# Performance work log

Measured on AMD Instinct MI355X. Metric: run time of the kernel, lower is better.

## Reference

```python
import jax, jax.numpy as jnp
import numpy as np

B, N, NS, D, H = 32, 4096, 16, 512, 8
DH = D // H          # dims_per_head = 64
DFF = 4 * D          # ff_mlp hidden
SCALE = DH ** -0.5
EPS = 1e-8           # slot-attention renorm eps
LN_EPS = 1e-5        # torch LayerNorm default
ITERS = 3


def layer_norm(x, g, b):
    mu = jnp.mean(x, axis=-1, keepdims=True)
    var = jnp.mean((x - mu) ** 2, axis=-1, keepdims=True)
    return (x - mu) * jax.lax.rsqrt(var + LN_EPS) * g + b


def setup_inputs() -> dict:
    key = jax.random.key(0)
    ks = jax.random.split(key, 8)
    s = 0.02
    return {
        "inputs": jax.random.normal(ks[0], (B, N, D), jnp.float32),
        "conditioning": jax.random.normal(ks[1], (B, NS, D), jnp.float32),
        # norm_input
        "ln_in_g": jnp.ones((D,), jnp.float32),
        "ln_in_b": jnp.zeros((D,), jnp.float32),
        # projections (no bias: use_projection_bias=False)
        "Wk": jax.random.normal(ks[2], (D, D), jnp.float32) * s,
        "Wv": jax.random.normal(ks[3], (D, D), jnp.float32) * s,
        "Wq": jax.random.normal(ks[4], (D, D), jnp.float32) * s,
        "Wo": jax.random.normal(ks[5], (D, D), jnp.float32) * s,
        # norm_slots / norm_slots_ff_mlp
        "ln_s_g": jnp.ones((D,), jnp.float32),
        "ln_s_b": jnp.zeros((D,), jnp.float32),
        "ln_f_g": jnp.ones((D,), jnp.float32),
        "ln_f_b": jnp.zeros((D,), jnp.float32),
        # ff_mlp: Linear(D,4D) -> ReLU -> Linear(4D,D)
        "W1": jax.random.normal(ks[6], (D, DFF), jnp.float32) * s,
        "b1": jnp.zeros((DFF,), jnp.float32),
        "W2": jax.random.normal(ks[7], (DFF, D), jnp.float32) * s,
        "b2": jnp.zeros((D,), jnp.float32),
    }


def reference(inputs, conditioning, ln_in_g, ln_in_b, Wk, Wv, Wq, Wo,
              ln_s_g, ln_s_b, ln_f_g, ln_f_b, W1, b1, W2, b2):
    b = inputs.shape[0]
    x = layer_norm(inputs, ln_in_g, ln_in_b)                 # [b, n, D]
    k = (x @ Wk.T).reshape(b, N, H, DH)                      # [b, n, h, dh]
    v = (x @ Wv.T).reshape(b, N, H, DH)

    slots = conditioning
    attn_mean = None
    for _ in range(ITERS):
        slots_prev = slots
        s = layer_norm(slots, ln_s_g, ln_s_b)
        q = (s @ Wq.T).reshape(b, NS, H, DH)                 # [b, ns, h, dh]
        dots = jnp.einsum("bihd,bjhd->bihj", q, k) * SCALE   # [b, ns, h, n]
        # softmax over flattened (slots, heads) axis, per input location j
        attn = jax.nn.softmax(dots.reshape(b, NS * H, N), axis=1)
        attn = attn.reshape(b, NS, H, N)
        attn_before = attn
        attn = attn + EPS
        attn = attn / jnp.sum(attn, axis=-1, keepdims=True)  # renorm over j
        updates = jnp.einsum("bjhd,bihj->bihd", v, attn)     # [b, ns, h, dh]
        updates = updates.reshape(b, NS, D)
        slots = updates @ Wo.T + slots_prev                  # to_o + residual
        slots_prev_ff = slots
        s2 = layer_norm(slots, ln_f_g, ln_f_b)
        s2 = jax.nn.relu(s2 @ W1 + b1) @ W2 + b2             # ff_mlp
        slots = s2 + slots_prev_ff
        attn_mean = jnp.mean(attn_before, axis=2)            # [b, ns, n]
    return slots, attn_mean
```

## Files before the change

kernel.cpp:

```cpp
#include <hip/hip_runtime.h>
#include <cstdint>
#include <cstddef>

typedef __attribute__((ext_vector_type(8))) short short8;
typedef __attribute__((ext_vector_type(4))) short short4v;
typedef __attribute__((ext_vector_type(8))) __bf16 bf16x8;
typedef __attribute__((ext_vector_type(4))) float f32x4;
typedef unsigned short u16;

static constexpr int Bb = 32, Nn = 4096, NSs = 16, Dd = 512, Hh = 8, DFF = 2048;
static constexpr float SCALE = 0.125f;
static constexpr float EPSR  = 1e-8f;
static constexpr float LN_EPS = 1e-5f;

__device__ __forceinline__ u16 f2b(float x) {
  union { float f; uint32_t u; } a; a.f = x;
  uint32_t r = a.u + 0x7fffu + ((a.u >> 16) & 1u);
  return (u16)(r >> 16);
}

__device__ __forceinline__ f32x4 mfma16(short8 a, short8 b, f32x4 c) {
  return __builtin_amdgcn_mfma_f32_16x16x32_bf16(
      __builtin_bit_cast(bf16x8, a), __builtin_bit_cast(bf16x8, b), c, 0, 0, 0);
}

__device__ __forceinline__ void gload16(const u16* g, u16* l) {
  __builtin_amdgcn_global_load_lds(
      (const __attribute__((address_space(1))) void*)g,
      (__attribute__((address_space(3))) void*)l, 16, 0, 0);
}

__global__ __launch_bounds__(256) void ln_rows(const float* __restrict__ src,
    const float* __restrict__ g, const float* __restrict__ bt,
    u16* __restrict__ dst, int R) {
  int row = blockIdx.x * 4 + (threadIdx.x >> 6);
  if (row >= R) return;
  int lane = threadIdx.x & 63;
  const float* p = src + (size_t)row * Dd + lane * 8;
  float4 u0 = *(const float4*)p;
  float4 u1 = *(const float4*)(p + 4);
  float x[8] = {u0.x,u0.y,u0.z,u0.w,u1.x,u1.y,u1.z,u1.w};
  float s = 0.f, s2 = 0.f;
#pragma unroll
  for (int e = 0; e < 8; ++e) { s += x[e]; s2 += x[e]*x[e]; }
#pragma unroll
  for (int m = 1; m < 64; m <<= 1) { s += __shfl_xor(s, m); s2 += __shfl_xor(s2, m); }
  float mean = s * (1.f/512.f);
  float var  = s2 * (1.f/512.f) - mean*mean;
  float rstd = rsqrtf(var + LN_EPS);
  union { u16 o[8]; short8 v; } ou;
#pragma unroll
  for (int e = 0; e < 8; ++e)
    ou.o[e] = f2b((x[e]-mean)*rstd*g[lane*8+e] + bt[lane*8+e]);
  *(short8*)(dst + (size_t)row * Dd + lane * 8) = ou.v;
}

__global__ __launch_bounds__(256, 2) void gemm_kv(const u16* __restrict__ A,
    const u16* __restrict__ Bk, const u16* __restrict__ Bv,
    u16* __restrict__ Ck, u16* __restrict__ CvT) {
  __shared__ u16 lA[128*32];
  __shared__ u16 lK[128*32];
  __shared__ u16 lV[128*32];
  const int tid = threadIdx.x, lane = tid & 63, wid = tid >> 6;
  const int wr = wid >> 1, wc = wid & 1;
  const int bm = blockIdx.y * 128, bn = blockIdx.x * 128;
  const size_t BN = (size_t)Bb * Nn;
  f32x4 ak[4][4] = {};
  f32x4 av[4][4] = {};
  const int srow = wid*16 + (lane >> 2), scol = (lane & 3) * 8;
  const u16* Ap = A  + (size_t)(bm + srow) * Dd + scol;
  const u16* Kp = Bk + (size_t)(bn + srow) * Dd + scol;
  const u16* Vp = Bv + (size_t)(bn + srow) * Dd + scol;
  u16* lAd = &lA[wid * 512];
  u16* lKd = &lK[wid * 512];
  u16* lVd = &lV[wid * 512];
  const int li = lane & 15, lk = lane >> 4;
  for (int k0 = 0; k0 < Dd; k0 += 32) {
    __syncthreads();
    gload16(Ap + k0, lAd);
    gload16(Ap + (size_t)64*Dd + k0, lAd + 2048);
    gload16(Kp + k0, lKd);
    gload16(Kp + (size_t)64*Dd + k0, lKd + 2048);
    gload16(Vp + k0, lVd);
    gload16(Vp + (size_t)64*Dd + k0, lVd + 2048);
    __syncthreads();
    short8 af[4], kf[4], vf[4];
#pragma unroll
    for (int m = 0; m < 4; ++m)
      af[m] = *(const short8*)&lA[(wr*64 + m*16 + li)*32 + lk*8];
#pragma unroll
    for (int n = 0; n < 4; ++n) {
      kf[n] = *(const short8*)&lK[(wc*64 + n*16 + li)*32 + lk*8];
      vf[n] = *(const short8*)&lV[(wc*64 + n*16 + li)*32 + lk*8];
    }
#pragma unroll
    for (int m = 0; m < 4; ++m)
#pragma unroll
      for (int n = 0; n < 4; ++n) {
        ak[m][n] = mfma16(af[m], kf[n], ak[m][n]);
        av[m][n] = mfma16(af[m], vf[n], av[m][n]);
      }
  }
  const int lr = lk * 4;
#pragma unroll
  for (int m = 0; m < 4; ++m)
#pragma unroll
    for (int n = 0; n < 4; ++n) {
      int row = bm + wr*64 + m*16 + lr;
      int col = bn + wc*64 + n*16 + li;
      f32x4 vk = ak[m][n];
#pragma unroll
      for (int r = 0; r < 4; ++r)
        Ck[(size_t)(row + r) * Dd + col] = f2b(vk[r]);
      f32x4 vv = av[m][n];
      union { u16 o[4]; short4v v4; } ou;
#pragma unroll
      for (int r = 0; r < 4; ++r) ou.o[r] = f2b(vv[r]);
      *(short4v*)&CvT[(size_t)col * BN + row] = ou.v4;
    }
}

template<int EP>
__global__ __launch_bounds__(256) void gemm64(const u16* __restrict__ A,
    const u16* __restrict__ Bw, void* __restrict__ Cp,
    const float* __restrict__ bias, const float* __restrict__ res,
    int N, int K) {
  __shared__ u16 lA[64*32];
  __shared__ u16 lB[64*32];
  const int tid = threadIdx.x, lane = tid & 63, wid = tid >> 6;
  const int wr = wid >> 1, wc = wid & 1;
  const int bm = blockIdx.y * 64, bn = blockIdx.x * 64;
  f32x4 acc[2][2] = {};
  const int srow = wid*16 + (lane >> 2), scol = (lane & 3) * 8;
  const u16* Ap = A + (size_t)(bm + srow) * K + scol;
  const u16* Bp = Bw + (size_t)(bn + srow) * K + scol;
  u16* lAd = &lA[wid * 512];
  u16* lBd = &lB[wid * 512];
  const int li = lane & 15, lk = lane >> 4;
  for (int k0 = 0; k0 < K; k0 += 32) {
    __syncthreads();
    gload16(Ap + k0, lAd);
    gload16(Bp + k0, lBd);
    __syncthreads();
    short8 af[2], bf[2];
#pragma unroll
    for (int m = 0; m < 2; ++m)
      af[m] = *(const short8*)&lA[(wr*32 + m*16 + li)*32 + lk*8];
#pragma unroll
    for (int n = 0; n < 2; ++n)
      bf[n] = *(const short8*)&lB[(wc*32 + n*16 + li)*32 + lk*8];
#pragma unroll
    for (int m = 0; m < 2; ++m)
#pragma unroll
      for (int n = 0; n < 2; ++n)
        acc[m][n] = mfma16(af[m], bf[n], acc[m][n]);
  }
  const int lr = lk * 4;
#pragma unroll
  for (int m = 0; m < 2; ++m)
#pragma unroll
    for (int n = 0; n < 2; ++n) {
      int row = bm + wr*32 + m*16 + lr;
      int col = bn + wc*32 + n*16 + li;
      f32x4 v = acc[m][n];
#pragma unroll
      for (int r = 0; r < 4; ++r) {
        size_t off = (size_t)(row + r) * N + col;
        float x = v[r];
        if constexpr (EP == 0) ((u16*)Cp)[off] = f2b(x);
        else if constexpr (EP == 1) ((float*)Cp)[off] = x + res[off];
        else if constexpr (EP == 2) { x += bias[col]; ((u16*)Cp)[off] = f2b(x > 0.f ? x : 0.f); }
        else ((float*)Cp)[off] = x + bias[col] + res[off];
      }
    }
}

__global__ __launch_bounds__(256) void attn_a(const u16* __restrict__ q,
    const u16* __restrict__ kk, u16* __restrict__ attnb,
    float* __restrict__ rowsum, float* __restrict__ attn_mean) {
  const int jt = blockIdx.x, b = blockIdx.y;
  const int tid = threadIdx.x, lane = tid & 63, wid = tid >> 6;
  __shared__ float sc[64][129];
  __shared__ float red[4][64];
  const int li = lane & 15, lk = lane >> 4;
#pragma unroll
  for (int hh = 0; hh < 2; ++hh) {
    const int h = wid * 2 + hh;
    const u16* qb = q + (((size_t)b*16 + li)*8 + h)*64 + lk*8;
    short8 a0 = *(const short8*)qb;
    short8 a1 = *(const short8*)(qb + 32);
#pragma unroll
    for (int n = 0; n < 4; ++n) {
      const u16* kb = kk + ((size_t)b*Nn + jt*64 + n*16 + li)*Dd + h*64 + lk*8;
      f32x4 acc = {};
      acc = mfma16(a0, *(const short8*)kb, acc);
      acc = mfma16(a1, *(const short8*)(kb + 32), acc);
#pragma unroll
      for (int r = 0; r < 4; ++r)
        sc[n*16 + li][(lk*4 + r)*8 + h] = acc[r] * SCALE;
    }
  }
  __syncthreads();
  const int jl = tid & 63, qt = tid >> 6;
  float mx = -1e30f;
#pragma unroll
  for (int e = 0; e < 32; ++e) mx = fmaxf(mx, sc[jl][qt*32 + e]);
  red[qt][jl] = mx;
  __syncthreads();
  float M = fmaxf(fmaxf(red[0][jl], red[1][jl]), fmaxf(red[2][jl], red[3][jl]));
  __syncthreads();
  float s = 0.f;
#pragma unroll
  for (int e = 0; e < 32; ++e) {
    float ev = __expf(sc[jl][qt*32 + e] - M);
    sc[jl][qt*32 + e] = ev; s += ev;
  }
  red[qt][jl] = s;
  __syncthreads();
  float S = red[0][jl] + red[1][jl] + red[2][jl] + red[3][jl];
  float inv = 1.f / S;
#pragma unroll
  for (int e = 0; e < 32; ++e)
    sc[jl][qt*32 + e] = sc[jl][qt*32 + e] * inv + EPSR;
  __syncthreads();
  if (tid < 128) {
    float rs = 0.f;
    for (int j2 = 0; j2 < 64; ++j2) rs += sc[j2][tid];
    atomicAdd(&rowsum[b*128 + tid], rs);
  }
#pragma unroll
  for (int e = 0; e < 32; ++e) {
    int r = qt*32 + e;
    attnb[((size_t)b*128 + r)*Nn + jt*64 + jl] = f2b(sc[jl][r]);
  }
  if (attn_mean != nullptr && tid < 64) {
    for (int i = 0; i < 16; ++i) {
      float sm = 0.f;
#pragma unroll
      for (int h = 0; h < 8; ++h) sm += sc[tid][i*8 + h];
      attn_mean[((size_t)b*16 + i)*Nn + jt*64 + tid] = sm * 0.125f - EPSR;
    }
  }
}

__global__ __launch_bounds__(256) void attn_b(const u16* __restrict__ attnb,
    const u16* __restrict__ vT, const float* __restrict__ rowsum,
    u16* __restrict__ upd) {
  const int h = blockIdx.x, b = blockIdx.y;
  const int lane = threadIdx.x & 63, wid = threadIdx.x >> 6;
  const int li = lane & 15, lk = lane >> 4;
  const size_t BN = (size_t)Bb * Nn;
  const u16* Ap = attnb + ((size_t)b*128 + li*8 + h)*Nn + lk*8;
  const u16* Bp = vT + (size_t)(h*64 + wid*16 + li)*BN + (size_t)b*Nn + lk*8;
  f32x4 acc[4] = {};
  for (int k0 = 0; k0 < Nn; k0 += 128) {
#pragma unroll
    for (int e = 0; e < 4; ++e)
      acc[e] = mfma16(*(const short8*)(Ap + k0 + e*32),
                      *(const short8*)(Bp + k0 + e*32), acc[e]);
  }
#pragma unroll
  for (int r = 0; r < 4; ++r) {
    int i = lk*4 + r;
    float t = acc[0][r] + acc[1][r] + acc[2][r] + acc[3][r];
    float rs = rowsum[b*128 + i*8 + h];
    upd[((size_t)b*16 + i)*Dd + h*64 + wid*16 + li] = f2b(t / rs);
  }
}

__global__ void cvt_w(const float* __restrict__ s, u16* __restrict__ d, int n) {
  int i = blockIdx.x*256 + threadIdx.x;
  if (i < n) d[i] = f2b(s[i]);
}
__global__ __launch_bounds__(256) void tr_cvt(const float* __restrict__ s,
    u16* __restrict__ d, int R, int C) {
  __shared__ u16 t[32][33];
  const int c0 = blockIdx.x*32, r0 = blockIdx.y*32;
  const int tr = threadIdx.x >> 3, tc4 = (threadIdx.x & 7)*4;
  float4 v = *(const float4*)&s[(size_t)(r0+tr)*C + c0 + tc4];
  t[tr][tc4+0] = f2b(v.x); t[tr][tc4+1] = f2b(v.y);
  t[tr][tc4+2] = f2b(v.z); t[tr][tc4+3] = f2b(v.w);
  __syncthreads();
  const int oc = threadIdx.x >> 3, or4 = (threadIdx.x & 7)*4;
  union { u16 o[4]; short4v v4; } ou;
#pragma unroll
  for (int e = 0; e < 4; ++e) ou.o[e] = t[or4+e][oc];
  *(short4v*)&d[(size_t)(c0+oc)*R + r0 + or4] = ou.v4;
}
__global__ void copy_f32v4(const float* __restrict__ s, float* __restrict__ d, int n4) {
  int i = blockIdx.x*256 + threadIdx.x;
  if (i < n4) ((float4*)d)[i] = ((const float4*)s)[i];
}

extern "C" void kernel_launch(void* const* d_in, const int* in_sizes, int n_in,
                              void* d_out, int out_size, void* d_ws, size_t ws_size,
                              hipStream_t stream) {
  (void)in_sizes; (void)n_in; (void)out_size; (void)ws_size;
  const float* inputs  = (const float*)d_in[0];
  const float* cond    = (const float*)d_in[1];
  const float* ln_in_g = (const float*)d_in[2];
  const float* ln_in_b = (const float*)d_in[3];
  const float* Wk = (const float*)d_in[4];
  const float* Wv = (const float*)d_in[5];
  const float* Wq = (const float*)d_in[6];
  const float* Wo = (const float*)d_in[7];
  const float* ln_s_g = (const float*)d_in[8];
  const float* ln_s_b = (const float*)d_in[9];
  const float* ln_f_g = (const float*)d_in[10];
  const float* ln_f_b = (const float*)d_in[11];
  const float* W1 = (const float*)d_in[12];
  const float* b1 = (const float*)d_in[13];
  const float* W2 = (const float*)d_in[14];
  const float* b2 = (const float*)d_in[15];
  float* out_slots = (float*)d_out;
  float* out_amean = (float*)d_out + (size_t)Bb*NSs*Dd;

  char* w = (char*)d_ws;
  auto alloc = [&](size_t bytes) {
    char* p = w; w += (bytes + 255) & ~(size_t)255; return p;
  };
  u16*  xn    = (u16*)alloc((size_t)Bb*Nn*Dd*2);
  u16*  kbuf  = (u16*)alloc((size_t)Bb*Nn*Dd*2);
  u16*  vT    = (u16*)alloc((size_t)Bb*Nn*Dd*2);
  u16*  attnb = (u16*)alloc((size_t)Bb*128*Nn*2);
  float* slots = (float*)alloc((size_t)Bb*NSs*Dd*4);
  u16*  qb    = (u16*)alloc((size_t)Bb*NSs*Dd*2);
  u16*  snb   = (u16*)alloc((size_t)Bb*NSs*Dd*2);
  u16*  s2nb  = (u16*)alloc((size_t)Bb*NSs*Dd*2);
  u16*  h1b   = (u16*)alloc((size_t)Bb*NSs*DFF*2);
  u16*  updb  = (u16*)alloc((size_t)Bb*NSs*Dd*2);
  float* rowsum = (float*)alloc((size_t)Bb*128*3*4);
  u16*  wkb = (u16*)alloc(262144*2);
  u16*  wvb = (u16*)alloc(262144*2);
  u16*  wqb = (u16*)alloc(262144*2);
  u16*  wob = (u16*)alloc(262144*2);
  u16*  w1t = (u16*)alloc((size_t)1048576*2);
  u16*  w2t = (u16*)alloc((size_t)1048576*2);

  cvt_w<<<1024, 256, 0, stream>>>(Wk, wkb, 262144);
  cvt_w<<<1024, 256, 0, stream>>>(Wv, wvb, 262144);
  cvt_w<<<1024, 256, 0, stream>>>(Wq, wqb, 262144);
  cvt_w<<<1024, 256, 0, stream>>>(Wo, wob, 262144);
  tr_cvt<<<dim3(64, 16), 256, 0, stream>>>(W1, w1t, 512, 2048);
  tr_cvt<<<dim3(16, 64), 256, 0, stream>>>(W2, w2t, 2048, 512);
  copy_f32v4<<<256, 256, 0, stream>>>(cond, slots, 65536);
  hipMemsetAsync(rowsum, 0, (size_t)Bb*128*3*4, stream);
  ln_rows<<<Bb*Nn/4, 256, 0, stream>>>(inputs, ln_in_g, ln_in_b, xn, Bb*Nn);
  gemm_kv<<<dim3(4, Bb*Nn/128), 256, 0, stream>>>(xn, wkb, wvb, kbuf, vT);

  for (int it = 0; it < 3; ++it) {
    float* rs = rowsum + (size_t)it * Bb * 128;
    ln_rows<<<128, 256, 0, stream>>>(slots, ln_s_g, ln_s_b, snb, Bb*NSs);
    gemm64<0><<<dim3(8, 8), 256, 0, stream>>>(snb, wqb, qb, nullptr, nullptr, 512, 512);
    attn_a<<<dim3(Nn/64, Bb), 256, 0, stream>>>(qb, kbuf, attnb, rs,
                                                it == 2 ? out_amean : nullptr);
    attn_b<<<dim3(Hh, Bb), 256, 0, stream>>>(attnb, vT, rs, updb);
    gemm64<1><<<dim3(8, 8), 256, 0, stream>>>(updb, wob, slots, nullptr, slots, 512, 512);
    ln_rows<<<128, 256, 0, stream>>>(slots, ln_f_g, ln_f_b, s2nb, Bb*NSs);
    gemm64<2><<<dim3(32, 8), 256, 0, stream>>>(s2nb, w1t, h1b, b1, nullptr, 2048, 512);
    gemm64<3><<<dim3(8, 8), 256, 0, stream>>>(h1b, w2t, slots, b2, slots, 512, 2048);
  }
  copy_f32v4<<<256, 256, 0, stream>>>(slots, out_slots, 65536);
}
```

Measured before the change: 726.7 us.

## Double-buffer LDS tiles in GEMMs and swizzle gemm_kv block order

Both the fused K/V projection GEMM and the generic 64x64 GEMM now use two LDS buffers per operand. The next K-slice is loaded while the current one feeds the MFMAs, so each iteration needs one barrier instead of two. This is meant to hide global-load latency behind matrix math, at the cost of doubled shared memory per block. gemm_kv also remaps its linear block index so that consecutive blocks on the same XCD share A rows and K/V weight tiles, aiming for better L2 reuse.

```diff
diff --git a/kernel.cpp b/kernel.cpp
--- a/kernel.cpp
+++ b/kernel.cpp
@@ -58,12 +58,14 @@
 __global__ __launch_bounds__(256, 2) void gemm_kv(const u16* __restrict__ A,
     const u16* __restrict__ Bk, const u16* __restrict__ Bv,
     u16* __restrict__ Ck, u16* __restrict__ CvT) {
-  __shared__ u16 lA[128*32];
-  __shared__ u16 lK[128*32];
-  __shared__ u16 lV[128*32];
+  __shared__ u16 lA[2][128*32];
+  __shared__ u16 lK[2][128*32];
+  __shared__ u16 lV[2][128*32];
   const int tid = threadIdx.x, lane = tid & 63, wid = tid >> 6;
   const int wr = wid >> 1, wc = wid & 1;
-  const int bm = blockIdx.y * 128, bn = blockIdx.x * 128;
+  const int n  = blockIdx.y * 4 + blockIdx.x;
+  const int orig = (n & 7) * 512 + (n >> 3);
+  const int bm = (orig >> 2) * 128, bn = (orig & 3) * 128;
   const size_t BN = (size_t)Bb * Nn;
   f32x4 ak[4][4] = {};
   f32x4 av[4][4] = {};
@@ -71,48 +73,57 @@
   const u16* Ap = A  + (size_t)(bm + srow) * Dd + scol;
   const u16* Kp = Bk + (size_t)(bn + srow) * Dd + scol;
   const u16* Vp = Bv + (size_t)(bn + srow) * Dd + scol;
-  u16* lAd = &lA[wid * 512];
-  u16* lKd = &lK[wid * 512];
-  u16* lVd = &lV[wid * 512];
+  const int ldb = wid * 512;
   const int li = lane & 15, lk = lane >> 4;
-  for (int k0 = 0; k0 < Dd; k0 += 32) {
+  gload16(Ap, &lA[0][ldb]);
+  gload16(Ap + (size_t)64*Dd, &lA[0][ldb + 2048]);
+  gload16(Kp, &lK[0][ldb]);
+  gload16(Kp + (size_t)64*Dd, &lK[0][ldb + 2048]);
+  gload16(Vp, &lV[0][ldb]);
+  gload16(Vp + (size_t)64*Dd, &lV[0][ldb + 2048]);
+  int cur = 0;
+  for (int t = 0; t < 16; ++t) {
     __syncthreads();
-    gload16(Ap + k0, lAd);
-    gload16(Ap + (size_t)64*Dd + k0, lAd + 2048);
-    gload16(Kp + k0, lKd);
-    gload16(Kp + (size_t)64*Dd + k0, lKd + 2048);
-    gload16(Vp + k0, lVd);
-    gload16(Vp + (size_t)64*Dd + k0, lVd + 2048);
-    __syncthreads();
+    const int nx = cur ^ 1;
+    if (t < 15) {
+      const int k0 = (t + 1) * 32;
+      gload16(Ap + k0, &lA[nx][ldb]);
+      gload16(Ap + (size_t)64*Dd + k0, &lA[nx][ldb + 2048]);
+      gload16(Kp + k0, &lK[nx][ldb]);
+      gload16(Kp + (size_t)64*Dd + k0, &lK[nx][ldb + 2048]);
+      gload16(Vp + k0, &lV[nx][ldb]);
+      gload16(Vp + (size_t)64*Dd + k0, &lV[nx][ldb + 2048]);
+    }
     short8 af[4], kf[4], vf[4];
 #pragma unroll
     for (int m = 0; m < 4; ++m)
-      af[m] = *(const short8*)&lA[(wr*64 + m*16 + li)*32 + lk*8];
-#pragma unroll
-    for (int n = 0; n < 4; ++n) {
-      kf[n] = *(const short8*)&lK[(wc*64 + n*16 + li)*32 + lk*8];
-      vf[n] = *(const short8*)&lV[(wc*64 + n*16 + li)*32 + lk*8];
+      af[m] = *(const short8*)&lA[cur][(wr*64 + m*16 + li)*32 + lk*8];
+#pragma unroll
+    for (int nn2 = 0; nn2 < 4; ++nn2) {
+      kf[nn2] = *(const short8*)&lK[cur][(wc*64 + nn2*16 + li)*32 + lk*8];
+      vf[nn2] = *(const short8*)&lV[cur][(wc*64 + nn2*16 + li)*32 + lk*8];
     }
 #pragma unroll
     for (int m = 0; m < 4; ++m)
 #pragma unroll
-      for (int n = 0; n < 4; ++n) {
-        ak[m][n] = mfma16(af[m], kf[n], ak[m][n]);
-        av[m][n] = mfma16(af[m], vf[n], av[m][n]);
+      for (int nn2 = 0; nn2 < 4; ++nn2) {
+        ak[m][nn2] = mfma16(af[m], kf[nn2], ak[m][nn2]);
+        av[m][nn2] = mfma16(af[m], vf[nn2], av[m][nn2]);
       }
+    cur = nx;
   }
   const int lr = lk * 4;
 #pragma unroll
   for (int m = 0; m < 4; ++m)
 #pragma unroll
-    for (int n = 0; n < 4; ++n) {
+    for (int nn2 = 0; nn2 < 4; ++nn2) {
       int row = bm + wr*64 + m*16 + lr;
-      int col = bn + wc*64 + n*16 + li;
-      f32x4 vk = ak[m][n];
+      int col = bn + wc*64 + nn2*16 + li;
+      f32x4 vk = ak[m][nn2];
 #pragma unroll
       for (int r = 0; r < 4; ++r)
         Ck[(size_t)(row + r) * Dd + col] = f2b(vk[r]);
-      f32x4 vv = av[m][n];
+      f32x4 vv = av[m][nn2];
       union { u16 o[4]; short4v v4; } ou;
 #pragma unroll
       for (int r = 0; r < 4; ++r) ou.o[r] = f2b(vv[r]);
@@ -125,8 +136,8 @@
     const u16* __restrict__ Bw, void* __restrict__ Cp,
     const float* __restrict__ bias, const float* __restrict__ res,
     int N, int K) {
-  __shared__ u16 lA[64*32];
-  __shared__ u16 lB[64*32];
+  __shared__ u16 lA[2][64*32];
+  __shared__ u16 lB[2][64*32];
   const int tid = threadIdx.x, lane = tid & 63, wid = tid >> 6;
   const int wr = wid >> 1, wc = wid & 1;
   const int bm = blockIdx.y * 64, bn = blockIdx.x * 64;
@@ -134,35 +145,42 @@
   const int srow = wid*16 + (lane >> 2), scol = (lane & 3) * 8;
   const u16* Ap = A + (size_t)(bm + srow) * K + scol;
   const u16* Bp = Bw + (size_t)(bn + srow) * K + scol;
-  u16* lAd = &lA[wid * 512];
-  u16* lBd = &lB[wid * 512];
+  const int ldb = wid * 512;
   const int li = lane & 15, lk = lane >> 4;
-  for (int k0 = 0; k0 < K; k0 += 32) {
+  const int nsteps = K >> 5;
+  gload16(Ap, &lA[0][ldb]);
+  gload16(Bp, &lB[0][ldb]);
+  int cur = 0;
+  for (int t = 0; t < nsteps; ++t) {
     __syncthreads();
-    gload16(Ap + k0, lAd);
-    gload16(Bp + k0, lBd);
-    __syncthreads();
+    const int nx = cur ^ 1;
+    if (t + 1 < nsteps) {
+      const int k0 = (t + 1) * 32;
+      gload16(Ap + k0, &lA[nx][ldb]);
+      gload16(Bp + k0, &lB[nx][ldb]);
+    }
     short8 af[2], bf[2];
 #pragma unroll
     for (int m = 0; m < 2; ++m)
-      af[m] = *(const short8*)&lA[(wr*32 + m*16 + li)*32 + lk*8];
-#pragma unroll
-    for (int n = 0; n < 2; ++n)
-      bf[n] = *(const short8*)&lB[(wc*32 + n*16 + li)*32 + lk*8];
+      af[m] = *(const short8*)&lA[cur][(wr*32 + m*16 + li)*32 + lk*8];
+#pragma unroll
+    for (int nn2 = 0; nn2 < 2; ++nn2)
+      bf[nn2] = *(const short8*)&lB[cur][(wc*32 + nn2*16 + li)*32 + lk*8];
 #pragma unroll
     for (int m = 0; m < 2; ++m)
 #pragma unroll
-      for (int n = 0; n < 2; ++n)
-        acc[m][n] = mfma16(af[m], bf[n], acc[m][n]);
+      for (int nn2 = 0; nn2 < 2; ++nn2)
+        acc[m][nn2] = mfma16(af[m], bf[nn2], acc[m][nn2]);
+    cur = nx;
   }
   const int lr = lk * 4;
 #pragma unroll
   for (int m = 0; m < 2; ++m)
 #pragma unroll
-    for (int n = 0; n < 2; ++n) {
+    for (int nn2 = 0; nn2 < 2; ++nn2) {
       int row = bm + wr*32 + m*16 + lr;
-      int col = bn + wc*32 + n*16 + li;
-      f32x4 v = acc[m][n];
+      int col = bn + wc*32 + nn2*16 + li;
+      f32x4 v = acc[m][nn2];
 #pragma unroll
       for (int r = 0; r < 4; ++r) {
         size_t off = (size_t)(row + r) * N + col;
```

Result: no change. 726.1 us (-0.1%).
